# Performance work log

Measured on AMD Instinct MI355X. Metric: run time of the kernel, lower is better.

## Reference

```python
import jax, jax.numpy as jnp
import numpy as np

N = 100000       # nodes
E = 1600000      # edges
NFEAT = 256
NHID = 128
NCLASS = 1


def setup_inputs() -> dict:
    key = jax.random.key(0)
    ks = jax.random.split(key, 9)
    x = jax.random.normal(ks[0], (N, NFEAT), dtype=jnp.float32)
    src = jax.random.randint(ks[1], (E,), 0, N, dtype=jnp.int32)
    dst = jax.random.randint(ks[2], (E,), 0, N, dtype=jnp.int32)
    W1 = jax.random.normal(ks[3], (NFEAT, NHID), dtype=jnp.float32) * (1.0 / np.sqrt(NFEAT))
    b1 = jnp.zeros((NHID,), dtype=jnp.float32)
    W2 = jax.random.normal(ks[4], (NHID, NHID), dtype=jnp.float32) * (1.0 / np.sqrt(NHID))
    b2 = jnp.zeros((NHID,), dtype=jnp.float32)
    Wfc = jax.random.normal(ks[5], (NHID, NCLASS), dtype=jnp.float32) * (1.0 / np.sqrt(NHID))
    bfc = jnp.zeros((NCLASS,), dtype=jnp.float32)
    return {"x": x, "W1": W1, "b1": b1, "W2": W2, "b2": b2,
            "Wfc": Wfc, "bfc": bfc, "src": src, "dst": dst}


def reference(x, W1, b1, W2, b2, Wfc, bfc, src, dst):
    # Symmetric GCN normalization (DGL GraphConv, norm='both').
    ones = jnp.ones((E,), dtype=jnp.float32)
    out_deg = jax.ops.segment_sum(ones, src, num_segments=N)
    in_deg = jax.ops.segment_sum(ones, dst, num_segments=N)
    norm_s = jnp.maximum(out_deg, 1.0) ** -0.5  # [N] src-side norm
    norm_d = jnp.maximum(in_deg, 1.0) ** -0.5   # [N] dst-side norm

    def gconv(h, W, b):
        # weight-before-aggregate (math-equivalent; minimizes [E, d] gather width)
        m = (h * norm_s[:, None]) @ W          # [N, out]
        agg = jax.ops.segment_sum(m[src], dst, num_segments=N)  # SpMM via gather+scatter-add
        return agg * norm_d[:, None] + b

    h1 = jax.nn.relu(gconv(x, W1, b1))
    # dropout is identity in eval mode
    h2 = gconv(h1, W2, b2)
    return h2 @ Wfc + bfc  # [N, NCLASS]
```

## Files before the change

### kernel.cpp

```cpp
#include <hip/hip_runtime.h>
#include <hip/hip_bf16.h>

#define NNODES 100000
#define NEDGES 1600000
#define NF 256
#define NH 128
#define SCAN_ELEMS 1024
#define SCAN_NBLK ((NNODES + SCAN_ELEMS - 1) / SCAN_ELEMS)

#define HG 200
#define HCHUNK (NEDGES / HG)
#define HBINS 50000
#define HR 2
#define HWORDS (NNODES / 2)

#define WPREP_BLOCKS 129

typedef _Float16 half4v __attribute__((ext_vector_type(4)));
typedef _Float16 half8v __attribute__((ext_vector_type(8)));
typedef float floatx16 __attribute__((ext_vector_type(16)));

__device__ __forceinline__ int pos16(int k) {
    return (((k >> 2) & 1) << 3) + (k & 3) + (((k >> 3) & 1) << 2);
}
__device__ __forceinline__ int ipos16(int p) {
    int g = (p >> 3) & 1, j = p & 7;
    return g * 4 + (j & 3) + ((j >> 2) << 3);
}

__device__ __forceinline__ float2 h2f2(unsigned u) {
    union { unsigned u; _Float16 h[2]; } c; c.u = u;
    return make_float2((float)c.h[0], (float)c.h[1]);
}

__device__ __forceinline__ void load_lds16(const void* g, void* l) {
    __builtin_amdgcn_global_load_lds(
        (const __attribute__((address_space(1))) void*)g,
        (__attribute__((address_space(3))) void*)l, 16, 0, 0);
}

__global__ __launch_bounds__(512)
void hist_part_kernel(const int* __restrict__ src, const int* __restrict__ dst,
                      unsigned* __restrict__ partial) {
    __shared__ unsigned lds[HBINS / 2];
    const int g = blockIdx.x, t = threadIdx.x;
    const int e0 = g * HCHUNK;
    for (int r = 0; r < HR; ++r) {
        const int lo = r * HBINS;
        for (int i = t; i < HBINS / 2; i += 512) lds[i] = 0;
        __syncthreads();
        for (int i = t; i < HCHUNK; i += 512) {
            unsigned us = (unsigned)(src[e0 + i] - lo);
            if (us < HBINS) atomicAdd(&lds[us >> 1], 1u << ((us & 1) * 16));
            unsigned ud = (unsigned)(dst[e0 + i] - lo);
            if (ud < HBINS) atomicAdd(&lds[ud >> 1], 1u << ((ud & 1) * 16 + 8));
        }
        __syncthreads();
        unsigned* dp = partial + (size_t)g * HWORDS + (lo >> 1);
        for (int i = t; i < HBINS / 2; i += 512) dp[i] = lds[i];
        __syncthreads();
    }
}

__global__ __launch_bounds__(256)
void degscan_kernel(const unsigned* __restrict__ partial,
                    unsigned char* __restrict__ offb,
                    float* __restrict__ ns, float* __restrict__ nd,
                    int* __restrict__ cnt_in) {
    int w = blockIdx.x * 256 + threadIdx.x;
    if (w >= HWORDS) return;
    unsigned o0 = 0, i0 = 0, o1 = 0, i1 = 0;
    for (int g0 = 0; g0 < HG; g0 += 8) {
        unsigned v[8];
        #pragma unroll
        for (int j = 0; j < 8; ++j) v[j] = partial[(size_t)(g0 + j) * HWORDS + w];
        #pragma unroll
        for (int j = 0; j < 8; ++j) {
            *(unsigned short*)(offb + (size_t)(g0 + j) * NNODES + 2 * w) =
                (unsigned short)((i0 & 0xffu) | ((i1 & 0xffu) << 8));
            o0 += v[j] & 0xffu;         i0 += (v[j] >> 8) & 0xffu;
            o1 += (v[j] >> 16) & 0xffu; i1 += v[j] >> 24;
        }
    }
    int n0 = 2 * w, n1 = 2 * w + 1;
    ns[n0] = rsqrtf((float)max((int)o0, 1));
    nd[n0] = rsqrtf((float)max((int)i0, 1));
    cnt_in[n0] = (int)i0;
    ns[n1] = rsqrtf((float)max((int)o1, 1));
    nd[n1] = rsqrtf((float)max((int)i1, 1));
    cnt_in[n1] = (int)i1;
}

__global__ __launch_bounds__(256)
void scanA_kernel(const int* __restrict__ cnt, int* __restrict__ pre,
                  int* __restrict__ bsum, int n) {
    __shared__ int tsum[256];
    int b = blockIdx.x, t = threadIdx.x;
    int base = b * SCAN_ELEMS + t * 4;
    int v[4]; int s = 0;
    #pragma unroll
    for (int k = 0; k < 4; ++k) { int idx = base + k; v[k] = (idx < n) ? cnt[idx] : 0; s += v[k]; }
    tsum[t] = s;
    __syncthreads();
    for (int off = 1; off < 256; off <<= 1) {
        int val = (t >= off) ? tsum[t - off] : 0;
        __syncthreads();
        tsum[t] += val;
        __syncthreads();
    }
    int run = (t == 0) ? 0 : tsum[t - 1];
    #pragma unroll
    for (int k = 0; k < 4; ++k) { int idx = base + k; if (idx < n) pre[idx] = run; run += v[k]; }
    if (t == 255) bsum[b] = tsum[255];
}

__global__ __launch_bounds__(128)
void scanB_kernel(int* __restrict__ bsum, int nb, int* __restrict__ row_ptr) {
    __shared__ int s[128];
    int t = threadIdx.x;
    int v = (t < nb) ? bsum[t] : 0;
    s[t] = v;
    __syncthreads();
    for (int off = 1; off < 128; off <<= 1) {
        int u = (t >= off) ? s[t - off] : 0;
        __syncthreads();
        s[t] += u;
        __syncthreads();
    }
    if (t < nb) bsum[t] = s[t] - v;
    if (t == 0) row_ptr[NNODES] = NEDGES;
}

__global__ __launch_bounds__(256)
void scanC_kernel(int* __restrict__ pre, const int* __restrict__ bsum, int n) {
    int add = bsum[blockIdx.x];
    int base = blockIdx.x * SCAN_ELEMS + threadIdx.x;
    #pragma unroll
    for (int k = 0; k < 4; ++k) {
        int idx = base + k * 256;
        if (idx < n) pre[idx] += add;
    }
}

__global__ __launch_bounds__(512)
void fill_kernel(const int* __restrict__ src, const int* __restrict__ dst,
                 const int* __restrict__ row_ptr, const unsigned char* __restrict__ offb,
                 int* __restrict__ col) {
    __shared__ unsigned lcur[HBINS / 2];
    const int g = blockIdx.x, t = threadIdx.x;
    const int e0 = g * HCHUNK;
    const unsigned char* ob = offb + (size_t)g * NNODES;
    for (int r = 0; r < HR; ++r) {
        const int lo = r * HBINS;
        for (int i = t; i < HBINS / 2; i += 512) lcur[i] = 0;
        __syncthreads();
        for (int i = t; i < HCHUNK; i += 512) {
            int d = dst[e0 + i];
            unsigned ud = (unsigned)(d - lo);
            if (ud < HBINS) {
                unsigned prev = atomicAdd(&lcur[ud >> 1], 1u << ((ud & 1) * 16));
                unsigned rank = (prev >> ((ud & 1) * 16)) & 0xffffu;
                int p = row_ptr[d] + (int)ob[d] + (int)rank;
                col[p] = src[e0 + i];
            }
        }
        __syncthreads();
    }
}

__global__ __launch_bounds__(256)
void prep_w_kernel(const float* __restrict__ W1, const float* __restrict__ b1,
                   _Float16* __restrict__ Wt1, float* __restrict__ b1p,
                   const float* __restrict__ W2, const float* __restrict__ Wfc,
                   const float* __restrict__ b2, const float* __restrict__ bfc,
                   float* __restrict__ v2p, float* __restrict__ c0) {
    int b = blockIdx.x, t = threadIdx.x;
    if (b < WPREP_BLOCKS) {
        int id = b * 256 + t;
        if (id < NF * NH) {
            int k = id >> 7, n = id & 127;
            Wt1[(size_t)n * NF + (k & ~15) + pos16(k & 15)] = (_Float16)W1[id];
        } else if (id < NF * NH + NH) {
            int pos = id - NF * NH;
            int k = (pos & ~15) + ipos16(pos & 15);
            b1p[pos] = b1[k];
        }
    } else {
        if (t < 128) {
            float s = 0.f;
            #pragma unroll 16
            for (int j = 0; j < 128; ++j) s += W2[t * 128 + j] * Wfc[j];
            v2p[(t & ~15) + pos16(t & 15)] = s;
        } else if (t < 192) {
            int lane = t - 128;
            float c = b2[lane] * Wfc[lane] + b2[lane + 64] * Wfc[lane + 64];
            #pragma unroll
            for (int off = 32; off > 0; off >>= 1) c += __shfl_down(c, off);
            if (lane == 0) c0[0] = c + bfc[0];
        }
    }
}

__global__ __launch_bounds__(128, 4)
void gemm1_kernel(const float* __restrict__ X, const _Float16* __restrict__ Wt,
                  const float* __restrict__ norm_s, _Float16* __restrict__ Cout,
                  int N) {
    __shared__ __align__(16) float As[2][64 * 32];
    const int tid = threadIdx.x;
    const int l = tid & 63, w = tid >> 6;
    const int wc = w;
    const int row0 = blockIdx.x * 64;

    const _Float16* Bb = Wt + (size_t)(wc * 64 + (l & 31)) * NF + (l >> 5) * 8;
    const int ar = l & 31;
    const int swz = ar & 7;
    const int g = l >> 5;
    const int lr = l >> 3, lc = l & 7;
    floatx16 acc[2][2] = {};

    #pragma unroll
    for (int i = 0; i < 4; ++i) {
        int R = w * 32 + i * 8;
        int r = R + lr;
        int grow = min(row0 + r, N - 1);
        int srcc = lc ^ (r & 7);
        load_lds16(X + (size_t)grow * NF + srcc * 4, &As[0][R * 32]);
    }

    for (int t = 0; t < 8; ++t) {
        const int cur = t & 1;
        if (t < 7) {
            #pragma unroll
            for (int i = 0; i < 4; ++i) {
                int R = w * 32 + i * 8;
                int r = R + lr;
                int grow = min(row0 + r, N - 1);
                int srcc = lc ^ (r & 7);
                load_lds16(X + (size_t)grow * NF + (t + 1) * 32 + srcc * 4,
                           &As[cur ^ 1][R * 32]);
            }
            __builtin_amdgcn_sched_barrier(0);
            asm volatile("s_waitcnt vmcnt(4)" ::: "memory");
            __builtin_amdgcn_sched_barrier(0);
        } else {
            __builtin_amdgcn_sched_barrier(0);
            asm volatile("s_waitcnt vmcnt(0)" ::: "memory");
            __builtin_amdgcn_sched_barrier(0);
        }
        __builtin_amdgcn_s_barrier();
        #pragma unroll
        for (int kk = 0; kk < 2; ++kk) {
            int ca = kk * 4 + g;
            int cb = ca + 2;
            float4 a0l = *(const float4*)&As[cur][(size_t)ar * 32 + (ca ^ swz) * 4];
            float4 a0h = *(const float4*)&As[cur][(size_t)ar * 32 + (cb ^ swz) * 4];
            float4 a1l = *(const float4*)&As[cur][(size_t)(ar + 32) * 32 + (ca ^ swz) * 4];
            float4 a1h = *(const float4*)&As[cur][(size_t)(ar + 32) * 32 + (cb ^ swz) * 4];
            half8v a0 = { (_Float16)a0l.x, (_Float16)a0l.y, (_Float16)a0l.z, (_Float16)a0l.w,
                          (_Float16)a0h.x, (_Float16)a0h.y, (_Float16)a0h.z, (_Float16)a0h.w };
            half8v a1 = { (_Float16)a1l.x, (_Float16)a1l.y, (_Float16)a1l.z, (_Float16)a1l.w,
                          (_Float16)a1h.x, (_Float16)a1h.y, (_Float16)a1h.z, (_Float16)a1h.w };
            const _Float16* bp = Bb + (t * 2 + kk) * 16;
            half8v b0 = *(const half8v*)bp;
            half8v b1 = *(const half8v*)(bp + (size_t)32 * NF);
            acc[0][0] = __builtin_amdgcn_mfma_f32_32x32x16_f16(a0, b0, acc[0][0], 0, 0, 0);
            acc[0][1] = __builtin_amdgcn_mfma_f32_32x32x16_f16(a0, b1, acc[0][1], 0, 0, 0);
            acc[1][0] = __builtin_amdgcn_mfma_f32_32x32x16_f16(a1, b0, acc[1][0], 0, 0, 0);
            acc[1][1] = __builtin_amdgcn_mfma_f32_32x32x16_f16(a1, b1, acc[1][1], 0, 0, 0);
        }
        __builtin_amdgcn_s_barrier();
    }

    const int cpos = pos16(l & 15);
    const int chi = ((l >> 4) & 1) << 4;
    #pragma unroll
    for (int m = 0; m < 2; ++m) {
        #pragma unroll
        for (int r = 0; r < 16; ++r) {
            int rloc = m * 32 + (r & 3) + ((r >> 2) << 3) + ((l >> 5) << 2);
            int grow = row0 + rloc;
            if (grow < N) {
                float s = norm_s[grow];
                #pragma unroll
                for (int n = 0; n < 2; ++n) {
                    int colbase = wc * 64 + n * 32 + chi;
                    Cout[(size_t)grow * NH + colbase + cpos] = (_Float16)(acc[m][n][r] * s);
                }
            }
        }
    }
}

__global__ __launch_bounds__(512)
void gatherz_kernel(const _Float16* __restrict__ m, const int* __restrict__ row_ptr,
                    const int* __restrict__ col, const float* __restrict__ norm_d,
                    const float* __restrict__ norm_s, const float* __restrict__ b1p,
                    const float* __restrict__ v2p, float* __restrict__ z, int N) {
    int w = (blockIdx.x * 512 + threadIdx.x) >> 6;
    int lane = threadIdx.x & 63;
    if (w >= N) return;
    int beg = __builtin_amdgcn_readfirstlane(row_ptr[w]);
    int end = __builtin_amdgcn_readfirstlane(row_ptr[w + 1]);
    const unsigned* mu = (const unsigned*)m + lane;
    float ax = 0.f, ay = 0.f;
    int i = beg;
    for (; i + 15 < end; i += 16) {
        unsigned u[16];
        #pragma unroll
        for (int j = 0; j < 16; ++j) u[j] = mu[(size_t)col[i + j] * 64];
        #pragma unroll
        for (int j = 0; j < 16; ++j) { float2 v = h2f2(u[j]); ax += v.x; ay += v.y; }
    }
    for (; i + 3 < end; i += 4) {
        unsigned u[4];
        #pragma unroll
        for (int j = 0; j < 4; ++j) u[j] = mu[(size_t)col[i + j] * 64];
        #pragma unroll
        for (int j = 0; j < 4; ++j) { float2 v = h2f2(u[j]); ax += v.x; ay += v.y; }
    }
    for (; i < end; ++i) {
        float2 v = h2f2(mu[(size_t)col[i] * 64]);
        ax += v.x; ay += v.y;
    }
    float nd = norm_d[w], ns = norm_s[w];
    float2 bv = ((const float2*)b1p)[lane];
    float hx = fmaxf(fmaf(ax, nd, bv.x), 0.f) * ns;
    float hy = fmaxf(fmaf(ay, nd, bv.y), 0.f) * ns;
    float2 w2 = ((const float2*)v2p)[lane];
    float p = fmaf(hx, w2.x, hy * w2.y);
    #pragma unroll
    for (int off = 32; off > 0; off >>= 1) p += __shfl_down(p, off);
    if (lane == 0) z[w] = p;
}

__global__ __launch_bounds__(256)
void outsum_kernel(const float* __restrict__ z, const int* __restrict__ row_ptr,
                   const int* __restrict__ col, const float* __restrict__ norm_d,
                   const float* __restrict__ c0, float* __restrict__ out, int N) {
    int w = blockIdx.x * 256 + threadIdx.x;
    if (w >= N) return;
    int beg = row_ptr[w], end = row_ptr[w + 1];
    float s0 = 0.f, s1 = 0.f, s2 = 0.f, s3 = 0.f;
    int i = beg;
    for (; i + 3 < end; i += 4) {
        s0 += z[col[i]];     s1 += z[col[i + 1]];
        s2 += z[col[i + 2]]; s3 += z[col[i + 3]];
    }
    for (; i < end; ++i) s0 += z[col[i]];
    out[w] = norm_d[w] * ((s0 + s1) + (s2 + s3)) + c0[0];
}

extern "C" void kernel_launch(void* const* d_in, const int* in_sizes, int n_in,
                              void* d_out, int out_size, void* d_ws, size_t ws_size,
                              hipStream_t stream) {
    const float* x   = (const float*)d_in[0];
    const float* W1  = (const float*)d_in[1];
    const float* b1  = (const float*)d_in[2];
    const float* W2  = (const float*)d_in[3];
    const float* b2  = (const float*)d_in[4];
    const float* Wfc = (const float*)d_in[5];
    const float* bfc = (const float*)d_in[6];
    const int*   src = (const int*)d_in[7];
    const int*   dst = (const int*)d_in[8];
    float* out = (float*)d_out;

    const int N = NNODES, E = NEDGES;

    char* p = (char*)d_ws;
    float*    norm_s = (float*)p;      p += (size_t)N * 4;
    float*    norm_d = (float*)p;      p += (size_t)N * 4;
    _Float16* bufA_h = (_Float16*)p;   p += (size_t)N * NH * 2;
    _Float16* Wt1    = (_Float16*)p;   p += (size_t)NF * NH * 2;
    float*    b1p    = (float*)p;      p += NH * 4;
    float*    v2p    = (float*)p;      p += NH * 4;
    float*    c0     = (float*)p;      p += 16;
    float*    z      = (float*)p;      p += (size_t)N * 4;
    int*      cnt_in = (int*)p;        p += (size_t)N * 4;
    int*      row_ptr= (int*)p;        p += (size_t)(N + 1) * 4 + 12;
    int*      col    = (int*)p;        p += (size_t)E * 4;
    int*      bsum   = (int*)p;        p += 128 * 4;
    unsigned* partial= (unsigned*)p;
    unsigned char* offb = (unsigned char*)bufA_h;

    hist_part_kernel<<<HG, 512, 0, stream>>>(src, dst, partial);
    degscan_kernel<<<(HWORDS + 255) / 256, 256, 0, stream>>>(partial, offb, norm_s, norm_d, cnt_in);
    scanA_kernel<<<SCAN_NBLK, 256, 0, stream>>>(cnt_in, row_ptr, bsum, N);
    scanB_kernel<<<1, 128, 0, stream>>>(bsum, SCAN_NBLK, row_ptr);
    scanC_kernel<<<SCAN_NBLK, 256, 0, stream>>>(row_ptr, bsum, N);
    fill_kernel<<<HG, 512, 0, stream>>>(src, dst, row_ptr, offb, col);
    prep_w_kernel<<<WPREP_BLOCKS + 1, 256, 0, stream>>>(W1, b1, Wt1, b1p,
                                                        W2, Wfc, b2, bfc, v2p, c0);

    gemm1_kernel<<<(N + 63) / 64, 128, 0, stream>>>(x, Wt1, norm_s, bufA_h, N);
    gatherz_kernel<<<((size_t)N * 64 + 511) / 512, 512, 0, stream>>>(
        bufA_h, row_ptr, col, norm_d, norm_s, b1p, v2p, z, N);
    outsum_kernel<<<(N + 255) / 256, 256, 0, stream>>>(z, row_ptr, col, norm_d, c0, out, N);
}
```

Measured before the change: 194.8 us.

## Record per-edge rank in histogram pass and simplify CSR fill to edge-parallel

The histogram kernel now keeps the value returned by the in-block LDS atomic for each dst edge and stores it as a per-edge 8-bit rank. The fill kernel no longer repeats the LDS atomic pass over 200 blocks with two rounds. It becomes a flat one-thread-per-edge scatter that computes the position from row_ptr, the per-block offset and the stored rank. This removes the serial LDS atomics and low parallelism of the fill pass, at the cost of an extra byte write and read per edge and a slower atomic-with-return in the histogram. The rank is taken from the 8-bit dst counter field, so it relies on per-block, per-node counts fitting in a byte, which the existing packed counter layout already assumes.

```diff
diff --git a/kernel.cpp b/kernel.cpp
--- a/kernel.cpp
+++ b/kernel.cpp
@@ -41,7 +41,7 @@
 
 __global__ __launch_bounds__(512)
 void hist_part_kernel(const int* __restrict__ src, const int* __restrict__ dst,
-                      unsigned* __restrict__ partial) {
+                      unsigned* __restrict__ partial, unsigned char* __restrict__ rank8) {
     __shared__ unsigned lds[HBINS / 2];
     const int g = blockIdx.x, t = threadIdx.x;
     const int e0 = g * HCHUNK;
@@ -53,7 +53,11 @@
             unsigned us = (unsigned)(src[e0 + i] - lo);
             if (us < HBINS) atomicAdd(&lds[us >> 1], 1u << ((us & 1) * 16));
             unsigned ud = (unsigned)(dst[e0 + i] - lo);
-            if (ud < HBINS) atomicAdd(&lds[ud >> 1], 1u << ((ud & 1) * 16 + 8));
+            if (ud < HBINS) {
+                unsigned sh = (ud & 1) * 16 + 8;
+                unsigned prev = atomicAdd(&lds[ud >> 1], 1u << sh);
+                rank8[e0 + i] = (unsigned char)((prev >> sh) & 0xffu);
+            }
         }
         __syncthreads();
         unsigned* dp = partial + (size_t)g * HWORDS + (lo >> 1);
@@ -142,30 +146,17 @@
     }
 }
 
-__global__ __launch_bounds__(512)
+__global__ __launch_bounds__(256)
 void fill_kernel(const int* __restrict__ src, const int* __restrict__ dst,
+                 const unsigned char* __restrict__ rank8,
                  const int* __restrict__ row_ptr, const unsigned char* __restrict__ offb,
-                 int* __restrict__ col) {
-    __shared__ unsigned lcur[HBINS / 2];
-    const int g = blockIdx.x, t = threadIdx.x;
-    const int e0 = g * HCHUNK;
-    const unsigned char* ob = offb + (size_t)g * NNODES;
-    for (int r = 0; r < HR; ++r) {
-        const int lo = r * HBINS;
-        for (int i = t; i < HBINS / 2; i += 512) lcur[i] = 0;
-        __syncthreads();
-        for (int i = t; i < HCHUNK; i += 512) {
-            int d = dst[e0 + i];
-            unsigned ud = (unsigned)(d - lo);
-            if (ud < HBINS) {
-                unsigned prev = atomicAdd(&lcur[ud >> 1], 1u << ((ud & 1) * 16));
-                unsigned rank = (prev >> ((ud & 1) * 16)) & 0xffffu;
-                int p = row_ptr[d] + (int)ob[d] + (int)rank;
-                col[p] = src[e0 + i];
-            }
-        }
-        __syncthreads();
-    }
+                 int* __restrict__ col, int E) {
+    int e = blockIdx.x * 256 + threadIdx.x;
+    if (e >= E) return;
+    int d = dst[e];
+    int g = e / HCHUNK;
+    int pos = row_ptr[d] + (int)offb[(size_t)g * NNODES + d] + (int)rank8[e];
+    col[pos] = src[e];
 }
 
 __global__ __launch_bounds__(256)
@@ -379,15 +370,16 @@
     int*      row_ptr= (int*)p;        p += (size_t)(N + 1) * 4 + 12;
     int*      col    = (int*)p;        p += (size_t)E * 4;
     int*      bsum   = (int*)p;        p += 128 * 4;
+    unsigned char* rank8 = (unsigned char*)p;  p += (size_t)E;
     unsigned* partial= (unsigned*)p;
     unsigned char* offb = (unsigned char*)bufA_h;
 
-    hist_part_kernel<<<HG, 512, 0, stream>>>(src, dst, partial);
+    hist_part_kernel<<<HG, 512, 0, stream>>>(src, dst, partial, rank8);
     degscan_kernel<<<(HWORDS + 255) / 256, 256, 0, stream>>>(partial, offb, norm_s, norm_d, cnt_in);
     scanA_kernel<<<SCAN_NBLK, 256, 0, stream>>>(cnt_in, row_ptr, bsum, N);
     scanB_kernel<<<1, 128, 0, stream>>>(bsum, SCAN_NBLK, row_ptr);
     scanC_kernel<<<SCAN_NBLK, 256, 0, stream>>>(row_ptr, bsum, N);
-    fill_kernel<<<HG, 512, 0, stream>>>(src, dst, row_ptr, offb, col);
+    fill_kernel<<<(E + 255) / 256, 256, 0, stream>>>(src, dst, rank8, row_ptr, offb, col, E);
     prep_w_kernel<<<WPREP_BLOCKS + 1, 256, 0, stream>>>(W1, b1, Wt1, b1p,
                                                         W2, Wfc, b2, bfc, v2p, c0);
 
```

Result: no change. 195.9 us (+0.6%).
